# Optimization experiments

Measured on AMD Instinct MI355X. Metric: run time of the kernel, lower is better.

## Reference

```python
import jax, jax.numpy as jnp
import numpy as np

B, S, H, D = 4, 1024, 20, 64
DM = H * D          # 1280 model dim
DF = 4 * DM         # 5120 ffn dim
EPS = 1e-5          # haiku LayerNorm default


def setup_inputs() -> dict:
    key = jax.random.key(0)
    ks = jax.random.split(key, 12)
    sc = 1.0 / np.sqrt(DM)
    return {
        "x": jax.random.normal(ks[0], (B, S, DM), jnp.float32),
        "ln1_scale": jnp.ones((DM,), jnp.float32),
        "ln1_offset": jnp.zeros((DM,), jnp.float32),
        "wq": jax.random.normal(ks[1], (DM, DM), jnp.float32) * sc,
        "bq": jnp.zeros((DM,), jnp.float32),
        "wk": jax.random.normal(ks[2], (DM, DM), jnp.float32) * sc,
        "bk": jnp.zeros((DM,), jnp.float32),
        "wv": jax.random.normal(ks[3], (DM, DM), jnp.float32) * sc,
        "bv": jnp.zeros((DM,), jnp.float32),
        "wo": jax.random.normal(ks[4], (DM, DM), jnp.float32) * sc,
        "bo": jnp.zeros((DM,), jnp.float32),
        "ln2_scale": jnp.ones((DM,), jnp.float32),
        "ln2_offset": jnp.zeros((DM,), jnp.float32),
        "fc1_w": jax.random.normal(ks[5], (DM, DF), jnp.float32) * sc,
        "fc1_b": jnp.zeros((DF,), jnp.float32),
        "fc2_w": jax.random.normal(ks[6], (DF, DM), jnp.float32) * (1.0 / np.sqrt(DF)),
        "fc2_b": jnp.zeros((DM,), jnp.float32),
    }


def _layer_norm(x, scale, offset):
    m = jnp.mean(x, axis=-1, keepdims=True)
    v = jnp.mean(jnp.square(x - m), axis=-1, keepdims=True)
    return (x - m) * jax.lax.rsqrt(v + EPS) * scale + offset


def reference(x, ln1_scale, ln1_offset, wq, bq, wk, bk, wv, bv, wo, bo,
              ln2_scale, ln2_offset, fc1_w, fc1_b, fc2_w, fc2_b):
    b, s, dm = x.shape
    # --- self-attention sub-block ---
    res = x
    h = _layer_norm(x, ln1_scale, ln1_offset)
    q = (h @ wq + bq).reshape(b, s, H, D)
    k = (h @ wk + bk).reshape(b, s, H, D)
    v = (h @ wv + bv).reshape(b, s, H, D)
    logits = jnp.einsum('bthd,bThd->bhtT', q, k) / jnp.sqrt(jnp.asarray(D, x.dtype))
    weights = jax.nn.softmax(logits, axis=-1)
    attn = jnp.einsum('bhtT,bThd->bthd', weights, v).reshape(b, s, dm)
    x = res + (attn @ wo + bo)
    # --- MLP sub-block ---
    res = x
    h = _layer_norm(x, ln2_scale, ln2_offset)
    h = jax.nn.gelu(h @ fc1_w + fc1_b, approximate=False)
    x = res + (h @ fc2_w + fc2_b)
    return x
```

## Files before the change

kernel.cpp:

```cpp
#include <hip/hip_runtime.h>
#include <hip/hip_bf16.h>

typedef __hip_bfloat16 bf16;
typedef __attribute__((ext_vector_type(8))) short short8;
typedef __attribute__((ext_vector_type(4))) float f32x4;
typedef __attribute__((ext_vector_type(4))) unsigned short u16x4;

#define DMODEL 1280
#define DFFN   5120
#define BATCH  4
#define SEQ    1024
#define NHEAD  20
#define HDIM   64
#define NROWS  (BATCH * SEQ)

#define GLDS(g, l) __builtin_amdgcn_global_load_lds(                            \
    (const __attribute__((address_space(1))) void*)(g),                         \
    (__attribute__((address_space(3))) void*)(l), 16, 0, 0)

__global__ __launch_bounds__(256) void transpose_cvt(
    const float* __restrict__ in, bf16* __restrict__ out, int K, int N)
{
    __shared__ float tile[32][33];
    const int n0 = blockIdx.x * 32;
    const int k0 = blockIdx.y * 32;
    const int tx = threadIdx.x;
    const int ty = threadIdx.y;
    for (int i = 0; i < 32; i += 8)
        tile[ty + i][tx] = in[(size_t)(k0 + ty + i) * N + (n0 + tx)];
    __syncthreads();
    for (int i = 0; i < 32; i += 8)
        out[(size_t)(n0 + ty + i) * K + (k0 + tx)] = __float2bfloat16(tile[tx][ty + i]);
}

__global__ __launch_bounds__(256) void transpose_cvt4(
    const float* __restrict__ s0, const float* __restrict__ s1,
    const float* __restrict__ s2, const float* __restrict__ s3,
    bf16* __restrict__ d0, bf16* __restrict__ d1,
    bf16* __restrict__ d2, bf16* __restrict__ d3)
{
    __shared__ float tile[32][33];
    const float* in;
    bf16* out;
    switch (blockIdx.z) {
        case 0: in = s0; out = d0; break;
        case 1: in = s1; out = d1; break;
        case 2: in = s2; out = d2; break;
        default: in = s3; out = d3; break;
    }
    const int n0 = blockIdx.x * 32;
    const int k0 = blockIdx.y * 32;
    const int tx = threadIdx.x;
    const int ty = threadIdx.y;
    for (int i = 0; i < 32; i += 8)
        tile[ty + i][tx] = in[(size_t)(k0 + ty + i) * DMODEL + (n0 + tx)];
    __syncthreads();
    for (int i = 0; i < 32; i += 8)
        out[(size_t)(n0 + ty + i) * DMODEL + (k0 + tx)] = __float2bfloat16(tile[tx][ty + i]);
}

__global__ __launch_bounds__(256) void pack_bias3(
    const float* __restrict__ a, const float* __restrict__ b,
    const float* __restrict__ c, float* __restrict__ o)
{
    const int i = blockIdx.x * 256 + threadIdx.x;
    if (i < DMODEL) {
        o[i] = a[i];
        o[DMODEL + i] = b[i];
        o[2 * DMODEL + i] = c[i];
    }
}

__global__ __launch_bounds__(256) void ln_bf16(
    const float* __restrict__ x, const float* __restrict__ sc,
    const float* __restrict__ of, bf16* __restrict__ out)
{
    const int row = blockIdx.x;
    const float* xr = x + (size_t)row * DMODEL;
    float v[5];
    float s = 0.f, s2 = 0.f;
    for (int i = 0; i < 5; ++i) {
        v[i] = xr[threadIdx.x + i * 256];
        s += v[i];
        s2 += v[i] * v[i];
    }
    for (int off = 1; off < 64; off <<= 1) {
        s  += __shfl_xor(s, off);
        s2 += __shfl_xor(s2, off);
    }
    __shared__ float red[2][4];
    const int wid = threadIdx.x >> 6;
    if ((threadIdx.x & 63) == 0) { red[0][wid] = s; red[1][wid] = s2; }
    __syncthreads();
    s  = red[0][0] + red[0][1] + red[0][2] + red[0][3];
    s2 = red[1][0] + red[1][1] + red[1][2] + red[1][3];
    const float mean = s * (1.0f / DMODEL);
    const float var  = s2 * (1.0f / DMODEL) - mean * mean;
    const float rstd = rsqrtf(var + 1e-5f);
    for (int i = 0; i < 5; ++i) {
        const int c = threadIdx.x + i * 256;
        const float y = (v[i] - mean) * rstd * sc[c] + of[c];
        out[(size_t)row * DMODEL + c] = __float2bfloat16(y);
    }
}

__global__ __launch_bounds__(256) void reduce2_ln(
    const float* __restrict__ P, const float* __restrict__ bias,
    const float* __restrict__ res, float* __restrict__ x1,
    const float* __restrict__ sc, const float* __restrict__ of,
    bf16* __restrict__ h2)
{
    const int row = blockIdx.x;
    const size_t base = (size_t)row * DMODEL;
    const int MN = NROWS * DMODEL;
    float v[5];
    float s = 0.f, s2 = 0.f;
    for (int i = 0; i < 5; ++i) {
        const int c = threadIdx.x + i * 256;
        const float val = P[base + c] + P[MN + base + c] + bias[c] + res[base + c];
        v[i] = val;
        x1[base + c] = val;
        s += val;
        s2 += val * val;
    }
    for (int off = 1; off < 64; off <<= 1) {
        s  += __shfl_xor(s, off);
        s2 += __shfl_xor(s2, off);
    }
    __shared__ float red[2][4];
    const int wid = threadIdx.x >> 6;
    if ((threadIdx.x & 63) == 0) { red[0][wid] = s; red[1][wid] = s2; }
    __syncthreads();
    s  = red[0][0] + red[0][1] + red[0][2] + red[0][3];
    s2 = red[1][0] + red[1][1] + red[1][2] + red[1][3];
    const float mean = s * (1.0f / DMODEL);
    const float var  = s2 * (1.0f / DMODEL) - mean * mean;
    const float rstd = rsqrtf(var + 1e-5f);
    for (int i = 0; i < 5; ++i) {
        const int c = threadIdx.x + i * 256;
        const float y = (v[i] - mean) * rstd * sc[c] + of[c];
        h2[base + c] = __float2bfloat16(y);
    }
}

template <int EPI>
__global__ __launch_bounds__(256, 4) void gemm_bf16(
    const bf16* __restrict__ A, const bf16* __restrict__ Bt,
    const float* __restrict__ bias,
    bf16* __restrict__ Cb, float* __restrict__ Cf,
    int M, int N, int K, int klen)
{
    __shared__ bf16 As[2][128][32];
    __shared__ bf16 Bs[2][128][32];
    const int m0 = blockIdx.x * 128;
    const int n0 = blockIdx.y * 128;
    const int z  = blockIdx.z;
    const int kbeg = z * klen;

    const int tid  = threadIdx.x;
    const int lane = tid & 63;
    const int wid  = tid >> 6;
    const int wm   = (wid >> 1) * 64;
    const int wn   = (wid & 1) * 64;
    const int l15  = lane & 15;
    const int lq   = lane >> 4;

    f32x4 acc[4][4];
    for (int i = 0; i < 4; ++i)
        for (int j = 0; j < 4; ++j)
            acc[i][j] = (f32x4){0.f, 0.f, 0.f, 0.f};

    const int srow = lane >> 2;
    const int cph  = lane & 3;
    const int cgl8 = (cph ^ (srow & 3)) * 8;
    const int lrow = wid * 16 + srow;
    const int lcol = cph * 8;

    const bf16* aT = A  + (size_t)(m0 + lrow) * K + kbeg + cgl8;
    const bf16* bT = Bt + (size_t)(n0 + lrow) * K + kbeg + cgl8;
    const size_t rstep = (size_t)64 * K;

    GLDS(aT,         &As[0][lrow][lcol]);
    GLDS(aT + rstep, &As[0][lrow + 64][lcol]);
    GLDS(bT,         &Bs[0][lrow][lcol]);
    GLDS(bT + rstep, &Bs[0][lrow + 64][lcol]);

    const int ca = (lq ^ (l15 & 3)) * 8;
    const int nIter = klen / 32;
    for (int it = 0; it < nIter; ++it) {
        const int buf = it & 1;
        __syncthreads();
        if (it + 1 < nIter) {
            const int k1 = (it + 1) * 32;
            GLDS(aT + k1,         &As[buf ^ 1][lrow][lcol]);
            GLDS(aT + k1 + rstep, &As[buf ^ 1][lrow + 64][lcol]);
            GLDS(bT + k1,         &Bs[buf ^ 1][lrow][lcol]);
            GLDS(bT + k1 + rstep, &Bs[buf ^ 1][lrow + 64][lcol]);
        }
        short8 af[4], bfr[4];
        for (int mt = 0; mt < 4; ++mt)
            af[mt] = *(const short8*)(&As[buf][wm + mt * 16 + l15][ca]);
        for (int nt = 0; nt < 4; ++nt)
            bfr[nt] = *(const short8*)(&Bs[buf][wn + nt * 16 + l15][ca]);
        for (int mt = 0; mt < 4; ++mt)
            for (int nt = 0; nt < 4; ++nt)
                acc[mt][nt] = __builtin_amdgcn_mfma_f32_16x16x32_bf16(
                    af[mt], bfr[nt], acc[mt][nt], 0, 0, 0);
    }

    float* Pf = Cf + (size_t)z * M * N;
    for (int mt = 0; mt < 4; ++mt)
        for (int nt = 0; nt < 4; ++nt)
            for (int r = 0; r < 4; ++r) {
                const int row = m0 + wm + mt * 16 + lq * 4 + r;
                const int col = n0 + wn + nt * 16 + l15;
                if (EPI == 0) {
                    const float v = acc[mt][nt][r] + bias[col];
                    Cb[(size_t)row * N + col] = __float2bfloat16(v);
                } else if (EPI == 2) {
                    const float v = acc[mt][nt][r] + bias[col];
                    const float g = 0.5f * v * (1.0f + erff(v * 0.70710678118654752f));
                    Cb[(size_t)row * N + col] = __float2bfloat16(g);
                } else {
                    Pf[(size_t)row * N + col] = acc[mt][nt][r];
                }
            }
}

__global__ __launch_bounds__(256) void reduce2(
    const float* __restrict__ P, const float* __restrict__ bias,
    const float* __restrict__ res, float* __restrict__ out, int MN, int N)
{
    const int i = (blockIdx.x * 256 + threadIdx.x) * 4;
    if (i >= MN) return;
    const float4 p0 = *(const float4*)(P + i);
    const float4 p1 = *(const float4*)(P + MN + i);
    const float4 r  = *(const float4*)(res + i);
    const float4 b  = *(const float4*)(bias + (i % N));
    float4 o;
    o.x = p0.x + p1.x + r.x + b.x;
    o.y = p0.y + p1.y + r.y + b.y;
    o.z = p0.z + p1.z + r.z + b.z;
    o.w = p0.w + p1.w + r.w + b.w;
    *(float4*)(out + i) = o;
}

__global__ __launch_bounds__(256) void flash_attn(
    const bf16* __restrict__ qb, const bf16* __restrict__ kb,
    const bf16* __restrict__ vb, bf16* __restrict__ ob, int ldq)
{
    __shared__ bf16 Ks[2][64][64];
    __shared__ bf16 Vt[64][64];
    __shared__ bf16 Ps[4][16][64];

    const int bh = blockIdx.y;
    const int b  = bh / NHEAD;
    const int hh = bh % NHEAD;
    const int q0 = blockIdx.x * 64;
    const int tid  = threadIdx.x;
    const int lane = tid & 63;
    const int wid  = tid >> 6;
    const int l15  = lane & 15;
    const int lq   = lane >> 4;
    const int key  = l15 & 7;

    short8 qf[2];
    {
        const bf16* qp = qb + (size_t)(b * SEQ + q0 + wid * 16 + l15) * ldq
                         + hh * HDIM + lq * 8;
        for (int kk = 0; kk < 2; ++kk) {
            union { short8 v; bf16 h[8]; } u;
            u.v = *(const short8*)(qp + kk * 32);
            for (int j = 0; j < 8; ++j)
                u.h[j] = __float2bfloat16(__bfloat162float(u.h[j]) * 0.125f);
            qf[kk] = u.v;
        }
    }

    f32x4 o[4];
    for (int dt = 0; dt < 4; ++dt) o[dt] = (f32x4){0.f, 0.f, 0.f, 0.f};
    float lsum = 0.f;

    const int krow  = wid * 8 + (lane >> 3);
    const int kcgl8 = ((lane & 7) ^ (krow & 7)) * 8;
    const int kcph8 = (lane & 7) * 8;
    const int vd0  = (tid & 15) * 4;
    const int vkv0 = (tid >> 4) * 4;

    const bf16* kBase = kb + (size_t)(b * SEQ + krow) * ldq + hh * HDIM + kcgl8;
    const bf16* vBase = vb + (size_t)(b * SEQ + vkv0) * ldq + hh * HDIM + vd0;

    GLDS(kBase,                    &Ks[0][krow][kcph8]);
    GLDS(kBase + (size_t)32 * ldq, &Ks[0][krow + 32][kcph8]);
    u16x4 vr[4];
    for (int j = 0; j < 4; ++j)
        vr[j] = *(const u16x4*)(vBase + (size_t)j * ldq);

    const int nIter = SEQ / 64;
    for (int it = 0; it < nIter; ++it) {
        const int buf = it & 1;
        __syncthreads();
        for (int i = 0; i < 4; ++i) {
            u16x4 w = { vr[0][i], vr[1][i], vr[2][i], vr[3][i] };
            const int p = ((vkv0 >> 3) ^ ((vd0 + i) & 7)) * 8 + (vkv0 & 7);
            *(u16x4*)(&Vt[vd0 + i][p]) = w;
        }
        __syncthreads();

        if (it + 1 < nIter) {
            const size_t off = (size_t)(it + 1) * 64 * ldq;
            GLDS(kBase + off,                    &Ks[buf ^ 1][krow][kcph8]);
            GLDS(kBase + off + (size_t)32 * ldq, &Ks[buf ^ 1][krow + 32][kcph8]);
            for (int j = 0; j < 4; ++j)
                vr[j] = *(const u16x4*)(vBase + off + (size_t)j * ldq);
        }

        for (int mt = 0; mt < 4; ++mt) {
            const bf16* kp = &Ks[buf][mt * 16 + l15][0];
            const short8 kf0 = *(const short8*)(kp + ((0 + lq) ^ key) * 8);
            const short8 kf1 = *(const short8*)(kp + ((4 + lq) ^ key) * 8);
            f32x4 a = (f32x4){0.f, 0.f, 0.f, 0.f};
            a = __builtin_amdgcn_mfma_f32_16x16x32_bf16(kf0, qf[0], a, 0, 0, 0);
            a = __builtin_amdgcn_mfma_f32_16x16x32_bf16(kf1, qf[1], a, 0, 0, 0);
            union { u16x4 v; bf16 h[4]; } pk;
            for (int r = 0; r < 4; ++r) {
                const float p = __expf(a[r]);
                lsum += p;
                pk.h[r] = __float2bfloat16(p);
            }
            const int pc = ((mt * 2 + (lq >> 1)) ^ key) * 8 + (lq & 1) * 4;
            *(u16x4*)(&Ps[wid][l15][pc]) = pk.v;
        }

        for (int kk = 0; kk < 2; ++kk) {
            const short8 pf = *(const short8*)(
                &Ps[wid][l15][((lq + 4 * kk) ^ key) * 8]);
            for (int dt = 0; dt < 4; ++dt) {
                const short8 vf = *(const short8*)(
                    &Vt[dt * 16 + l15][((lq + 4 * kk) ^ key) * 8]);
                o[dt] = __builtin_amdgcn_mfma_f32_16x16x32_bf16(
                    vf, pf, o[dt], 0, 0, 0);
            }
        }
    }

    lsum += __shfl_xor(lsum, 16);
    lsum += __shfl_xor(lsum, 32);
    const float inv_l = 1.0f / lsum;

    const size_t qrow = (size_t)(b * SEQ + q0 + wid * 16 + l15);
    for (int dt = 0; dt < 4; ++dt) {
        union { u16x4 v; bf16 h[4]; } w;
        for (int r = 0; r < 4; ++r)
            w.h[r] = __float2bfloat16(o[dt][r] * inv_l);
        *(u16x4*)(ob + qrow * DMODEL + hh * HDIM + dt * 16 + lq * 4) = w.v;
    }
}

extern "C" void kernel_launch(void* const* d_in, const int* in_sizes, int n_in,
                              void* d_out, int out_size, void* d_ws, size_t ws_size,
                              hipStream_t stream)
{
    (void)in_sizes; (void)n_in; (void)out_size; (void)ws_size;
    const float* x    = (const float*)d_in[0];
    const float* ln1s = (const float*)d_in[1];
    const float* ln1o = (const float*)d_in[2];
    const float* wq   = (const float*)d_in[3];
    const float* bq   = (const float*)d_in[4];
    const float* wk   = (const float*)d_in[5];
    const float* bk   = (const float*)d_in[6];
    const float* wv   = (const float*)d_in[7];
    const float* bv   = (const float*)d_in[8];
    const float* wo   = (const float*)d_in[9];
    const float* bo   = (const float*)d_in[10];
    const float* ln2s = (const float*)d_in[11];
    const float* ln2o = (const float*)d_in[12];
    const float* fc1w = (const float*)d_in[13];
    const float* fc1b = (const float*)d_in[14];
    const float* fc2w = (const float*)d_in[15];
    const float* fc2b = (const float*)d_in[16];
    float* out = (float*)d_out;

    char* wp = (char*)d_ws;
    auto alloc = [&](size_t n) { char* p = wp; wp += (n + 255) & ~(size_t)255; return p; };
    bf16*  wqkvt = (bf16*)alloc((size_t)3 * DMODEL * DMODEL * 2);
    bf16*  wot   = (bf16*)alloc((size_t)DMODEL * DMODEL * 2);
    bf16*  fc1t  = (bf16*)alloc((size_t)DFFN * DMODEL * 2);
    bf16*  fc2t  = (bf16*)alloc((size_t)DMODEL * DFFN * 2);
    float* bqkv  = (float*)alloc((size_t)3 * DMODEL * 4);
    char*  regA  = alloc((size_t)NROWS * DMODEL * 2
                       + (size_t)NROWS * 3 * DMODEL * 2
                       + (size_t)NROWS * DMODEL * 2);
    bf16*  h     = (bf16*)regA;
    bf16*  qkv   = (bf16*)(regA + (size_t)NROWS * DMODEL * 2);
    bf16*  attn  = (bf16*)(regA + (size_t)NROWS * 4 * DMODEL * 2);
    float* part  = (float*)regA;
    bf16*  h2    = (bf16*)alloc((size_t)NROWS * DMODEL * 2);
    bf16*  g     = (bf16*)alloc((size_t)NROWS * DFFN * 2);
    float* x1    = out;

    const dim3 tb(32, 8);
    transpose_cvt4<<<dim3(DMODEL / 32, DMODEL / 32, 4), tb, 0, stream>>>(
        wq, wk, wv, wo,
        wqkvt, wqkvt + (size_t)DMODEL * DMODEL, wqkvt + (size_t)2 * DMODEL * DMODEL, wot);
    transpose_cvt<<<dim3(DFFN / 32, DMODEL / 32), tb, 0, stream>>>(fc1w, fc1t, DMODEL, DFFN);
    transpose_cvt<<<dim3(DMODEL / 32, DFFN / 32), tb, 0, stream>>>(fc2w, fc2t, DFFN, DMODEL);
    pack_bias3<<<(DMODEL + 255) / 256, 256, 0, stream>>>(bq, bk, bv, bqkv);

    ln_bf16<<<NROWS, 256, 0, stream>>>(x, ln1s, ln1o, h);

    gemm_bf16<0><<<dim3(NROWS / 128, 3 * DMODEL / 128, 1), 256, 0, stream>>>(
        h, wqkvt, bqkv, qkv, nullptr, NROWS, 3 * DMODEL, DMODEL, DMODEL);

    flash_attn<<<dim3(SEQ / 64, BATCH * NHEAD), 256, 0, stream>>>(
        qkv, qkv + DMODEL, qkv + 2 * DMODEL, attn, 3 * DMODEL);

    gemm_bf16<3><<<dim3(NROWS / 128, DMODEL / 128, 2), 256, 0, stream>>>(
        attn, wot, nullptr, nullptr, part, NROWS, DMODEL, DMODEL, DMODEL / 2);
    reduce2_ln<<<NROWS, 256, 0, stream>>>(part, bo, x, x1, ln2s, ln2o, h2);

    gemm_bf16<2><<<dim3(NROWS / 128, DFFN / 128, 1), 256, 0, stream>>>(
        h2, fc1t, fc1b, g, nullptr, NROWS, DFFN, DMODEL, DMODEL);

    gemm_bf16<3><<<dim3(NROWS / 128, DMODEL / 128, 2), 256, 0, stream>>>(
        g, fc2t, nullptr, nullptr, part, NROWS, DMODEL, DFFN, DFFN / 2);
    reduce2<<<(NROWS * DMODEL / 4 + 255) / 256, 256, 0, stream>>>(
        part, fc2b, x1, out, NROWS * DMODEL, DMODEL);
}
```

Measured before the change: 482.8 us.

## Stage GEMM tiles through registers with two-deep prefetch instead of direct-to-LDS loads

Replaces the global_load_lds direct-to-LDS copies in the bf16 GEMM with vector global loads into registers. Tiles are fetched two k-steps ahead, written to the alternate LDS buffer while the current one is computed, and the loop is unrolled by two. Barriers now wait only on LDS counters, so global-load latency no longer stalls at every __syncthreads. The LDS swizzle changes to match the new two-threads-per-row store pattern, and launch bounds drop from 4 to 3 blocks per CU to leave room for the extra staging registers. This can reduce occupancy, and the loop assumes an even iteration count of at least two.

New measurement: 507.6 us. +5.1%, slower.

```diff
diff --git a/kernel.cpp b/kernel.cpp
--- a/kernel.cpp
+++ b/kernel.cpp
@@ -17,6 +17,10 @@
 #define GLDS(g, l) __builtin_amdgcn_global_load_lds(                            \
     (const __attribute__((address_space(1))) void*)(g),                         \
     (__attribute__((address_space(3))) void*)(l), 16, 0, 0)
+
+#define LGKM_BARRIER() do {                                                     \
+    __builtin_amdgcn_s_waitcnt(0xC07F);      \
+    __builtin_amdgcn_s_barrier(); } while (0)
 
 __global__ __launch_bounds__(256) void transpose_cvt(
     const float* __restrict__ in, bf16* __restrict__ out, int K, int N)
@@ -144,7 +148,7 @@
 }
 
 template <int EPI>
-__global__ __launch_bounds__(256, 4) void gemm_bf16(
+__global__ __launch_bounds__(256, 3) void gemm_bf16(
     const bf16* __restrict__ A, const bf16* __restrict__ Bt,
     const float* __restrict__ bias,
     bf16* __restrict__ Cb, float* __restrict__ Cf,
@@ -170,43 +174,70 @@
         for (int j = 0; j < 4; ++j)
             acc[i][j] = (f32x4){0.f, 0.f, 0.f, 0.f};
 
-    const int srow = lane >> 2;
-    const int cph  = lane & 3;
-    const int cgl8 = (cph ^ (srow & 3)) * 8;
-    const int lrow = wid * 16 + srow;
-    const int lcol = cph * 8;
-
-    const bf16* aT = A  + (size_t)(m0 + lrow) * K + kbeg + cgl8;
-    const bf16* bT = Bt + (size_t)(n0 + lrow) * K + kbeg + cgl8;
-    const size_t rstep = (size_t)64 * K;
-
-    GLDS(aT,         &As[0][lrow][lcol]);
-    GLDS(aT + rstep, &As[0][lrow + 64][lcol]);
-    GLDS(bT,         &Bs[0][lrow][lcol]);
-    GLDS(bT + rstep, &Bs[0][lrow + 64][lcol]);
-
-    const int ca = (lq ^ (l15 & 3)) * 8;
+    const int srow = tid >> 1;
+    const int sc0  = (tid & 1) * 2;
+    const int skey = (srow >> 1) & 3;
+    const int sp0  = (sc0 ^ skey) * 8;
+    const int sp1  = ((sc0 + 1) ^ skey) * 8;
+
+    const bf16* aS = A  + (size_t)(m0 + srow) * K + kbeg + sc0 * 8;
+    const bf16* bS = Bt + (size_t)(n0 + srow) * K + kbeg + sc0 * 8;
+
+    uint4 a0c0, a0c1, b0c0, b0c1;
+    uint4 a1c0, a1c1, b1c0, b1c1;
+
+#define LOADSET0(k0) do {                                                       \
+    a0c0 = *(const uint4*)(aS + (k0));  a0c1 = *(const uint4*)(aS + (k0) + 8);  \
+    b0c0 = *(const uint4*)(bS + (k0));  b0c1 = *(const uint4*)(bS + (k0) + 8);  \
+} while (0)
+#define LOADSET1(k0) do {                                                       \
+    a1c0 = *(const uint4*)(aS + (k0));  a1c1 = *(const uint4*)(aS + (k0) + 8);  \
+    b1c0 = *(const uint4*)(bS + (k0));  b1c1 = *(const uint4*)(bS + (k0) + 8);  \
+} while (0)
+#define WRITESET0(buf) do {                                                     \
+    *(uint4*)(&As[buf][srow][sp0]) = a0c0; *(uint4*)(&As[buf][srow][sp1]) = a0c1; \
+    *(uint4*)(&Bs[buf][srow][sp0]) = b0c0; *(uint4*)(&Bs[buf][srow][sp1]) = b0c1; \
+} while (0)
+#define WRITESET1(buf) do {                                                     \
+    *(uint4*)(&As[buf][srow][sp0]) = a1c0; *(uint4*)(&As[buf][srow][sp1]) = a1c1; \
+    *(uint4*)(&Bs[buf][srow][sp0]) = b1c0; *(uint4*)(&Bs[buf][srow][sp1]) = b1c1; \
+} while (0)
+
+    const int ca = (lq ^ ((l15 >> 1) & 3)) * 8;
+#define COMPUTE(buf) do {                                                       \
+    short8 af[4], bfr[4];                                                       \
+    for (int mt = 0; mt < 4; ++mt)                                              \
+        af[mt] = *(const short8*)(&As[buf][wm + mt * 16 + l15][ca]);            \
+    for (int nt = 0; nt < 4; ++nt)                                              \
+        bfr[nt] = *(const short8*)(&Bs[buf][wn + nt * 16 + l15][ca]);           \
+    for (int mt = 0; mt < 4; ++mt)                                              \
+        for (int nt = 0; nt < 4; ++nt)                                          \
+            acc[mt][nt] = __builtin_amdgcn_mfma_f32_16x16x32_bf16(              \
+                af[mt], bfr[nt], acc[mt][nt], 0, 0, 0);                         \
+} while (0)
+
     const int nIter = klen / 32;
-    for (int it = 0; it < nIter; ++it) {
-        const int buf = it & 1;
-        __syncthreads();
-        if (it + 1 < nIter) {
-            const int k1 = (it + 1) * 32;
-            GLDS(aT + k1,         &As[buf ^ 1][lrow][lcol]);
-            GLDS(aT + k1 + rstep, &As[buf ^ 1][lrow + 64][lcol]);
-            GLDS(bT + k1,         &Bs[buf ^ 1][lrow][lcol]);
-            GLDS(bT + k1 + rstep, &Bs[buf ^ 1][lrow + 64][lcol]);
-        }
-        short8 af[4], bfr[4];
-        for (int mt = 0; mt < 4; ++mt)
-            af[mt] = *(const short8*)(&As[buf][wm + mt * 16 + l15][ca]);
-        for (int nt = 0; nt < 4; ++nt)
-            bfr[nt] = *(const short8*)(&Bs[buf][wn + nt * 16 + l15][ca]);
-        for (int mt = 0; mt < 4; ++mt)
-            for (int nt = 0; nt < 4; ++nt)
-                acc[mt][nt] = __builtin_amdgcn_mfma_f32_16x16x32_bf16(
-                    af[mt], bfr[nt], acc[mt][nt], 0, 0, 0);
-    }
+    LOADSET0(0);
+    LOADSET1(32);
+    WRITESET0(0);
+    LGKM_BARRIER();
+
+    for (int it = 0; it + 2 <= nIter; it += 2) {
+        if (it + 2 < nIter) LOADSET0((it + 2) * 32);
+        WRITESET1(1);
+        COMPUTE(0);
+        LGKM_BARRIER();
+        if (it + 3 < nIter) LOADSET1((it + 3) * 32);
+        if (it + 2 < nIter) WRITESET0(0);
+        COMPUTE(1);
+        LGKM_BARRIER();
+    }
+
+#undef LOADSET0
+#undef LOADSET1
+#undef WRITESET0
+#undef WRITESET1
+#undef COMPUTE
 
     float* Pf = Cf + (size_t)z * M * N;
     for (int mt = 0; mt < 4; ++mt)
```
